# Performance work log

Hardware: AMD Instinct MI355X
Metric: run time of the kernel (lower is better)

Reference implementation:

```python
import jax, jax.numpy as jnp
import numpy as np

N = 8192
F_IN = 256
F_OUT = 64
NEG_SLOPE = 0.01


def setup_inputs() -> dict:
    key = jax.random.key(0)
    k1, k2, k3, k4 = jax.random.split(key, 4)
    h = jax.random.normal(k1, (N, F_IN), dtype=jnp.float32)
    adj = jax.random.randint(k2, (N, N), 0, 2).astype(jnp.float32)
    # xavier_uniform-scaled params
    W = jax.random.uniform(k3, (F_IN, F_OUT), jnp.float32, -1.0, 1.0) * np.sqrt(6.0 / (F_IN + F_OUT)).astype(np.float32)
    a = jax.random.uniform(k4, (2 * F_OUT, 1), jnp.float32, -1.0, 1.0) * np.sqrt(6.0 / (2 * F_OUT + 1)).astype(np.float32)
    return {"h": h, "adj": adj, "W": W, "a": a, "rel": 0}


def reference(h, adj, W, a, rel):
    # Wh: [N, F']
    Wh = h @ W
    # Decompose additive score: e_ij = LeakyReLU(a1.Wh_i + a2.Wh_j)
    # (equivalent to cat([Wh_i, Wh_j]) @ a, without the [N,N,2F'] tensor)
    a1 = a[:F_OUT, 0]
    a2 = a[F_OUT:, 0]
    f1 = Wh @ a1  # [N]
    f2 = Wh @ a2  # [N]
    e = jax.nn.leaky_relu(f1[:, None] + f2[None, :], NEG_SLOPE)  # [N, N]
    e = jnp.where(adj > 0, e, -jnp.inf)
    attention = jax.nn.softmax(e, axis=1)  # dropout is identity at eval time
    h_prime = attention @ Wh  # [N, F']
    return h_prime, attention
```

## Files before the change

### kernel.cpp

```cpp
#include <hip/hip_runtime.h>
#include <hip/hip_bf16.h>

#define N 8192
#define FIN 256
#define FOUT 64
#define NEG_SLOPE 0.01f
#define CHUNK 256
#define NCHUNK (N / CHUNK)
#define RB 32
#define MWORDS (NCHUNK * 4)

typedef float f32x4 __attribute__((ext_vector_type(4)));
typedef __bf16 bf16x8 __attribute__((ext_vector_type(8)));
typedef unsigned long long ull;

__device__ __forceinline__ float lk(float x) { return x >= 0.f ? x : NEG_SLOPE * x; }

__global__ __launch_bounds__(256) void gat_k1(const float* __restrict__ h,
                                              const float* __restrict__ W,
                                              const float* __restrict__ a,
                                              unsigned short* __restrict__ WhB,
                                              float* __restrict__ f1,
                                              float* __restrict__ f2) {
  __shared__ float Ws[FIN * FOUT];
  const int t = threadIdx.x;
  const int lane = t & 63;
  const int w = t >> 6;
  const size_t row0 = (size_t)blockIdx.x * 16;

  for (int i = t; i < FIN * FOUT / 4; i += 256)
    ((f32x4*)Ws)[i] = ((const f32x4*)W)[i];
  __syncthreads();

  const float* h0 = h + row0 * FIN;
  float acc[4] = {0.f, 0.f, 0.f, 0.f};
  #pragma unroll 4
  for (int c4 = 0; c4 < FIN; c4 += 4) {
    const f32x4 hv0 = *(const f32x4*)(h0 + (w + 0)  * FIN + c4);
    const f32x4 hv1 = *(const f32x4*)(h0 + (w + 4)  * FIN + c4);
    const f32x4 hv2 = *(const f32x4*)(h0 + (w + 8)  * FIN + c4);
    const f32x4 hv3 = *(const f32x4*)(h0 + (w + 12) * FIN + c4);
    #pragma unroll
    for (int j = 0; j < 4; ++j) {
      const float wv = Ws[(c4 + j) * FOUT + lane];
      acc[0] = fmaf(hv0[j], wv, acc[0]);
      acc[1] = fmaf(hv1[j], wv, acc[1]);
      acc[2] = fmaf(hv2[j], wv, acc[2]);
      acc[3] = fmaf(hv3[j], wv, acc[3]);
    }
  }

  const float a1k = a[lane];
  const float a2k = a[FOUT + lane];
  #pragma unroll
  for (int i = 0; i < 4; ++i) {
    const size_t row = row0 + (w + 4 * i);
    WhB[(((row >> 3) * 64) + lane) * 8 + (row & 7)] =
        __builtin_bit_cast(unsigned short, __float2bfloat16(acc[i]));
    float p1 = acc[i] * a1k, p2 = acc[i] * a2k;
    #pragma unroll
    for (int off = 32; off; off >>= 1) {
      p1 += __shfl_down(p1, off);
      p2 += __shfl_down(p2, off);
    }
    if (lane == 0) { f1[row] = p1; f2[row] = p2; }
  }
}

__global__ __launch_bounds__(512) void gat_k2a(const float* __restrict__ adj,
                                               const float* __restrict__ f1g,
                                               const float* __restrict__ f2g,
                                               ull* __restrict__ mskg,
                                               float* __restrict__ izg) {
  const int t = threadIdx.x;
  const int lane = t & 63;
  const int w = t >> 6;
  const int row = blockIdx.x * 8 + w;
  const float f1r = f1g[row];
  const f32x4* arow = (const f32x4*)(adj + (size_t)row * N);
  ull* mrow = mskg + (size_t)row * MWORDS;

  float s = 0.f;
  #pragma unroll 4
  for (int c = 0; c < NCHUNK; ++c) {
    const f32x4 v = __builtin_nontemporal_load(arow + c * 64 + lane);
    const f32x4 f = *(const f32x4*)&f2g[c * CHUNK + lane * 4];
    const ull b0 = __ballot(v.x > 0.f);
    const ull b1 = __ballot(v.y > 0.f);
    const ull b2 = __ballot(v.z > 0.f);
    const ull b3 = __ballot(v.w > 0.f);
    const ull bb = lane == 0 ? b0 : lane == 1 ? b1 : lane == 2 ? b2 : b3;
    if (lane < 4) mrow[c * 4 + lane] = bb;
    s += (v.x > 0.f) ? __expf(lk(f1r + f.x)) : 0.f;
    s += (v.y > 0.f) ? __expf(lk(f1r + f.y)) : 0.f;
    s += (v.z > 0.f) ? __expf(lk(f1r + f.z)) : 0.f;
    s += (v.w > 0.f) ? __expf(lk(f1r + f.w)) : 0.f;
  }
  #pragma unroll
  for (int off = 32; off; off >>= 1) s += __shfl_xor(s, off);
  if (lane == 0) izg[row] = 1.f / s;
}

__global__ __launch_bounds__(512) void gat_k2b(const ull* __restrict__ mskg,
                                               const float* __restrict__ f1g,
                                               const float* __restrict__ f2g,
                                               const float* __restrict__ izg,
                                               const unsigned short* __restrict__ WhB,
                                               float* __restrict__ att,
                                               float* __restrict__ hp) {
  __shared__ __align__(16) unsigned char attb[2][RB * CHUNK * 2];
  const int t = threadIdx.x;
  const int lane = t & 63;
  const int w = t >> 6;
  const int mt = w >> 2, nt = w & 3;
  const size_t row0 = (size_t)blockIdx.x * RB;

  float f1r_[4], z_[4];
  #pragma unroll
  for (int rr = 0; rr < 4; ++rr) {
    f1r_[rr] = f1g[row0 + 4 * w + rr];
    z_[rr]   = izg[row0 + 4 * w + rr];
  }

  f32x4 acc = {0.f, 0.f, 0.f, 0.f};

  #pragma unroll 2
  for (int c = 0; c < NCHUNK; ++c) {
    unsigned char* ab = attb[c & 1];
    const f32x4 f = *(const f32x4*)&f2g[c * CHUNK + lane * 4];
    #pragma unroll
    for (int rr = 0; rr < 4; ++rr) {
      const int r = 4 * w + rr;
      const ull* mrow = mskg + (row0 + r) * (size_t)MWORDS + c * 4;
      const ull b0 = mrow[0], b1 = mrow[1], b2 = mrow[2], b3 = mrow[3];
      f32x4 p;
      p.x = ((b0 >> lane) & 1ull) ? __expf(lk(f1r_[rr] + f.x)) * z_[rr] : 0.f;
      p.y = ((b1 >> lane) & 1ull) ? __expf(lk(f1r_[rr] + f.y)) * z_[rr] : 0.f;
      p.z = ((b2 >> lane) & 1ull) ? __expf(lk(f1r_[rr] + f.z)) * z_[rr] : 0.f;
      p.w = ((b3 >> lane) & 1ull) ? __expf(lk(f1r_[rr] + f.w)) * z_[rr] : 0.f;
      __builtin_nontemporal_store(p, (f32x4*)(att + (row0 + r) * (size_t)N + c * CHUNK + lane * 4));
      const ull pk =
          (ull)__builtin_bit_cast(unsigned short, __float2bfloat16(p.x)) |
          ((ull)__builtin_bit_cast(unsigned short, __float2bfloat16(p.y)) << 16) |
          ((ull)__builtin_bit_cast(unsigned short, __float2bfloat16(p.z)) << 32) |
          ((ull)__builtin_bit_cast(unsigned short, __float2bfloat16(p.w)) << 48);
      int byte = r * (CHUNK * 2) + lane * 8;
      byte ^= (r & 7) << 4;
      *(ull*)(ab + byte) = pk;
    }
    __syncthreads();
    #pragma unroll
    for (int s = 0; s < 8; ++s) {
      const int arow_ = mt * 16 + (lane & 15);
      int off = arow_ * (CHUNK * 2) + s * 64 + (lane >> 4) * 16;
      off ^= (arow_ & 7) << 4;
      const bf16x8 afrag = *(const bf16x8*)(ab + off);
      const int kg = c * 32 + s * 4 + (lane >> 4);
      const bf16x8 bfrag = *(const bf16x8*)(WhB + ((size_t)kg * 64 + nt * 16 + (lane & 15)) * 8);
      acc = __builtin_amdgcn_mfma_f32_16x16x32_bf16(afrag, bfrag, acc, 0, 0, 0);
    }
  }

  const int col = nt * 16 + (lane & 15);
  const int rbase = mt * 16 + (lane >> 4) * 4;
  #pragma unroll
  for (int q = 0; q < 4; ++q)
    hp[(row0 + rbase + q) * FOUT + col] = acc[q];
}

extern "C" void kernel_launch(void* const* d_in, const int* in_sizes, int n_in,
                              void* d_out, int out_size, void* d_ws, size_t ws_size,
                              hipStream_t stream) {
  const float* h   = (const float*)d_in[0];
  const float* adj = (const float*)d_in[1];
  const float* W   = (const float*)d_in[2];
  const float* a   = (const float*)d_in[3];

  float* hp  = (float*)d_out;
  float* att = hp + (size_t)N * FOUT;

  unsigned short* WhB = (unsigned short*)d_ws;
  float* f1 = (float*)((char*)d_ws + (size_t)N * FOUT * 2);
  float* f2 = f1 + N;
  float* iz = f2 + N;
  ull*   msk = (ull*)(iz + N);

  gat_k1 <<<N / 16, 256, 0, stream>>>(h, W, a, WhB, f1, f2);
  gat_k2a<<<N / 8, 512, 0, stream>>>(adj, f1, f2, msk, iz);
  gat_k2b<<<N / RB, 512, 0, stream>>>(msk, f1, f2, iz, WhB, att, hp);
}
```

Measured before the change: 521.2 us.

## Fuse mask/normalizer pass into attention kernel with LDS-resident row masks

Merges the two row kernels into one. Each block of 256 threads now handles 8 rows: it first reads adj, builds the bit masks and the softmax normalizers in shared memory, then writes attention and runs the bf16 MFMA product against Wh. This removes the global round trip of the mask and normalizer arrays and one kernel launch. In exchange, the 16-row MFMA tile is half padding with zero rows. Each block also streams the whole of Wh for only 8 rows, which raises L2 traffic and redundant matrix work.

```diff
diff --git a/kernel.cpp b/kernel.cpp
--- a/kernel.cpp
+++ b/kernel.cpp
@@ -7,8 +7,8 @@
 #define NEG_SLOPE 0.01f
 #define CHUNK 256
 #define NCHUNK (N / CHUNK)
-#define RB 32
-#define MWORDS (NCHUNK * 4)
+#define RB 8
+#define MW (NCHUNK * 4)
 
 typedef float f32x4 __attribute__((ext_vector_type(4)));
 typedef __bf16 bf16x8 __attribute__((ext_vector_type(8)));
@@ -67,72 +67,70 @@
   }
 }
 
-__global__ __launch_bounds__(512) void gat_k2a(const float* __restrict__ adj,
-                                               const float* __restrict__ f1g,
-                                               const float* __restrict__ f2g,
-                                               ull* __restrict__ mskg,
-                                               float* __restrict__ izg) {
+__global__ __launch_bounds__(256) void gat_k2(const float* __restrict__ adj,
+                                              const float* __restrict__ f1g,
+                                              const float* __restrict__ f2g,
+                                              const unsigned short* __restrict__ WhB,
+                                              float* __restrict__ att,
+                                              float* __restrict__ hp) {
+  __shared__ ull msks[RB][MW];
+  __shared__ __align__(16) unsigned char attb[2][16 * CHUNK * 2];
+  __shared__ float izs[RB], f1s[RB];
+
   const int t = threadIdx.x;
   const int lane = t & 63;
   const int w = t >> 6;
-  const int row = blockIdx.x * 8 + w;
-  const float f1r = f1g[row];
-  const f32x4* arow = (const f32x4*)(adj + (size_t)row * N);
-  ull* mrow = mskg + (size_t)row * MWORDS;
-
-  float s = 0.f;
-  #pragma unroll 4
-  for (int c = 0; c < NCHUNK; ++c) {
-    const f32x4 v = __builtin_nontemporal_load(arow + c * 64 + lane);
-    const f32x4 f = *(const f32x4*)&f2g[c * CHUNK + lane * 4];
-    const ull b0 = __ballot(v.x > 0.f);
-    const ull b1 = __ballot(v.y > 0.f);
-    const ull b2 = __ballot(v.z > 0.f);
-    const ull b3 = __ballot(v.w > 0.f);
-    const ull bb = lane == 0 ? b0 : lane == 1 ? b1 : lane == 2 ? b2 : b3;
-    if (lane < 4) mrow[c * 4 + lane] = bb;
-    s += (v.x > 0.f) ? __expf(lk(f1r + f.x)) : 0.f;
-    s += (v.y > 0.f) ? __expf(lk(f1r + f.y)) : 0.f;
-    s += (v.z > 0.f) ? __expf(lk(f1r + f.z)) : 0.f;
-    s += (v.w > 0.f) ? __expf(lk(f1r + f.w)) : 0.f;
-  }
-  #pragma unroll
-  for (int off = 32; off; off >>= 1) s += __shfl_xor(s, off);
-  if (lane == 0) izg[row] = 1.f / s;
-}
-
-__global__ __launch_bounds__(512) void gat_k2b(const ull* __restrict__ mskg,
-                                               const float* __restrict__ f1g,
-                                               const float* __restrict__ f2g,
-                                               const float* __restrict__ izg,
-                                               const unsigned short* __restrict__ WhB,
-                                               float* __restrict__ att,
-                                               float* __restrict__ hp) {
-  __shared__ __align__(16) unsigned char attb[2][RB * CHUNK * 2];
-  const int t = threadIdx.x;
-  const int lane = t & 63;
-  const int w = t >> 6;
-  const int mt = w >> 2, nt = w & 3;
   const size_t row0 = (size_t)blockIdx.x * RB;
 
-  float f1r_[4], z_[4];
+  for (int i = t; i < 1024; i += 256) {
+    ((unsigned int*)(attb[0] + 8 * CHUNK * 2))[i] = 0u;
+    ((unsigned int*)(attb[1] + 8 * CHUNK * 2))[i] = 0u;
+  }
+
   #pragma unroll
-  for (int rr = 0; rr < 4; ++rr) {
-    f1r_[rr] = f1g[row0 + 4 * w + rr];
-    z_[rr]   = izg[row0 + 4 * w + rr];
+  for (int rr = 0; rr < 2; ++rr) {
+    const int r = 2 * w + rr;
+    const float f1r = f1g[row0 + r];
+    const f32x4* arow = (const f32x4*)(adj + (row0 + r) * (size_t)N);
+    float s = 0.f;
+    #pragma unroll 4
+    for (int c = 0; c < NCHUNK; ++c) {
+      const f32x4 v = __builtin_nontemporal_load(arow + c * 64 + lane);
+      const f32x4 f = *(const f32x4*)&f2g[c * CHUNK + lane * 4];
+      const ull b0 = __ballot(v.x > 0.f);
+      const ull b1 = __ballot(v.y > 0.f);
+      const ull b2 = __ballot(v.z > 0.f);
+      const ull b3 = __ballot(v.w > 0.f);
+      const ull bb = lane == 0 ? b0 : lane == 1 ? b1 : lane == 2 ? b2 : b3;
+      if (lane < 4) msks[r][c * 4 + lane] = bb;
+      s += (v.x > 0.f) ? __expf(lk(f1r + f.x)) : 0.f;
+      s += (v.y > 0.f) ? __expf(lk(f1r + f.y)) : 0.f;
+      s += (v.z > 0.f) ? __expf(lk(f1r + f.z)) : 0.f;
+      s += (v.w > 0.f) ? __expf(lk(f1r + f.w)) : 0.f;
+    }
+    #pragma unroll
+    for (int off = 32; off; off >>= 1) s += __shfl_xor(s, off);
+    if (lane == 0) { izs[r] = 1.f / s; f1s[r] = f1r; }
+  }
+  __syncthreads();
+
+  float f1r_[2], z_[2];
+  #pragma unroll
+  for (int rr = 0; rr < 2; ++rr) {
+    f1r_[rr] = f1s[2 * w + rr];
+    z_[rr]   = izs[2 * w + rr];
   }
 
   f32x4 acc = {0.f, 0.f, 0.f, 0.f};
-
   #pragma unroll 2
   for (int c = 0; c < NCHUNK; ++c) {
     unsigned char* ab = attb[c & 1];
     const f32x4 f = *(const f32x4*)&f2g[c * CHUNK + lane * 4];
     #pragma unroll
-    for (int rr = 0; rr < 4; ++rr) {
-      const int r = 4 * w + rr;
-      const ull* mrow = mskg + (row0 + r) * (size_t)MWORDS + c * 4;
-      const ull b0 = mrow[0], b1 = mrow[1], b2 = mrow[2], b3 = mrow[3];
+    for (int rr = 0; rr < 2; ++rr) {
+      const int r = 2 * w + rr;
+      const ull b0 = msks[r][c * 4 + 0], b1 = msks[r][c * 4 + 1];
+      const ull b2 = msks[r][c * 4 + 2], b3 = msks[r][c * 4 + 3];
       f32x4 p;
       p.x = ((b0 >> lane) & 1ull) ? __expf(lk(f1r_[rr] + f.x)) * z_[rr] : 0.f;
       p.y = ((b1 >> lane) & 1ull) ? __expf(lk(f1r_[rr] + f.y)) * z_[rr] : 0.f;
@@ -150,22 +148,24 @@
     }
     __syncthreads();
     #pragma unroll
-    for (int s = 0; s < 8; ++s) {
-      const int arow_ = mt * 16 + (lane & 15);
-      int off = arow_ * (CHUNK * 2) + s * 64 + (lane >> 4) * 16;
+    for (int s8 = 0; s8 < 8; ++s8) {
+      const int arow_ = lane & 15;
+      int off = arow_ * (CHUNK * 2) + s8 * 64 + (lane >> 4) * 16;
       off ^= (arow_ & 7) << 4;
       const bf16x8 afrag = *(const bf16x8*)(ab + off);
-      const int kg = c * 32 + s * 4 + (lane >> 4);
-      const bf16x8 bfrag = *(const bf16x8*)(WhB + ((size_t)kg * 64 + nt * 16 + (lane & 15)) * 8);
+      const int kg = c * 32 + s8 * 4 + (lane >> 4);
+      const bf16x8 bfrag = *(const bf16x8*)(WhB + ((size_t)kg * 64 + w * 16 + (lane & 15)) * 8);
       acc = __builtin_amdgcn_mfma_f32_16x16x32_bf16(afrag, bfrag, acc, 0, 0, 0);
     }
   }
 
-  const int col = nt * 16 + (lane & 15);
-  const int rbase = mt * 16 + (lane >> 4) * 4;
-  #pragma unroll
-  for (int q = 0; q < 4; ++q)
-    hp[(row0 + rbase + q) * FOUT + col] = acc[q];
+  const int col = w * 16 + (lane & 15);
+  const int rbase = (lane >> 4) * 4;
+  if (rbase < RB) {
+    #pragma unroll
+    for (int q = 0; q < 4; ++q)
+      hp[(row0 + rbase + q) * FOUT + col] = acc[q];
+  }
 }
 
 extern "C" void kernel_launch(void* const* d_in, const int* in_sizes, int n_in,
@@ -182,10 +182,7 @@
   unsigned short* WhB = (unsigned short*)d_ws;
   float* f1 = (float*)((char*)d_ws + (size_t)N * FOUT * 2);
   float* f2 = f1 + N;
-  float* iz = f2 + N;
-  ull*   msk = (ull*)(iz + N);
 
-  gat_k1 <<<N / 16, 256, 0, stream>>>(h, W, a, WhB, f1, f2);
-  gat_k2a<<<N / 8, 512, 0, stream>>>(adj, f1, f2, msk, iz);
-  gat_k2b<<<N / RB, 512, 0, stream>>>(msk, f1, f2, iz, WhB, att, hp);
+  gat_k1<<<N / 16, 256, 0, stream>>>(h, W, a, WhB, f1, f2);
+  gat_k2<<<N / RB, 256, 0, stream>>>(adj, f1, f2, WhB, att, hp);
 }
```

Result: no change. 511.1 us (-1.9%).
